# Kernel tuning notes

Hardware: AMD Instinct MI355X
Metric: run time of the kernel (lower is better)

## Reference

```python
import jax, jax.numpy as jnp
import numpy as np

B, D, H1, H2 = 128, 1024, 512, 128


def setup_inputs() -> dict:
    key = jax.random.key(0)
    ks = jax.random.split(key, 5)
    x = jax.random.normal(ks[0], (B, D), dtype=jnp.float32)
    W1 = jax.random.normal(ks[1], (H1, D), dtype=jnp.float32)
    W2 = jax.random.normal(ks[2], (H2, H1), dtype=jnp.float32)
    W3 = jax.random.normal(ks[3], (H1, H2), dtype=jnp.float32)
    W4 = jax.random.normal(ks[4], (D, H1), dtype=jnp.float32)
    b1 = jnp.full((H1,), 0.1, dtype=jnp.float32)
    b2 = jnp.full((H2,), 0.1, dtype=jnp.float32)
    b3 = jnp.full((H1,), 0.1, dtype=jnp.float32)
    b4 = jnp.full((D,), 0.1, dtype=jnp.float32)
    return {"x": x, "W1": W1, "b1": b1, "W2": W2, "b2": b2,
            "W3": W3, "b3": b3, "W4": W4, "b4": b4}


def reference(x, W1, b1, W2, b2, W3, b3, W4, b4):
    # Forward: 4-layer sigmoid autoencoder (calculate_jacobian=True path).
    c1 = jax.nn.sigmoid(x @ W1.T + b1)    # [B, H1]
    c2 = jax.nn.sigmoid(c1 @ W2.T + b2)   # [B, H2]
    c3 = jax.nn.sigmoid(c2 @ W3.T + b3)   # [B, H1]
    recover = c3 @ W4.T + b4              # [B, D]
    # Per-sample Jacobian of recover w.r.t. x, vectorized:
    # diag(sigma') matmul == row-scale, so avoid explicit diag matrices.
    s1 = c1 * (1.0 - c1)                  # [B, H1]
    s2 = c2 * (1.0 - c2)                  # [B, H2]
    s3 = c3 * (1.0 - c3)                  # [B, H1]
    G1 = s1[:, :, None] * W1              # [B, H1, D]
    G2 = jnp.einsum('bi,ij,bjd->bid', s2, W2, G1)   # [B, H2, D]
    G3 = jnp.einsum('bj,ji,bid->bjd', s3, W3, G2)   # [B, H1, D]
    Jac = jnp.einsum('oj,bjd->bod', W4, G3)          # [B, D, D]
    return recover, c2, Jac
```

## Files before the change

kernel.cpp:

```cpp
#include <hip/hip_runtime.h>

#define NB  128
#define ND  1024
#define NH1 512
#define NH2 128

typedef __attribute__((ext_vector_type(8))) short    short8;
typedef __attribute__((ext_vector_type(8))) _Float16 half8;
typedef __attribute__((ext_vector_type(4))) float    f32x4;

__device__ __forceinline__ float sigm(float v) { return 1.0f / (1.0f + __expf(-v)); }

__device__ __forceinline__ void bsplit(float v, unsigned short& h, unsigned short& l) {
    unsigned hu = __float_as_uint(v) & 0xffff0000u;
    h = (unsigned short)(hu >> 16);
    float r = v - __uint_as_float(hu);
    l = (unsigned short)(__float_as_uint(r) >> 16);
}

template<int K, int COLS, bool SIG>
__global__ __launch_bounds__(256)
void fc_kernel(const float* __restrict__ X, const float* __restrict__ W,
               const float* __restrict__ bias, float* __restrict__ Cout,
               float* __restrict__ Sout) {
    int idx4 = blockIdx.x * 256 + threadIdx.x;
    int out = idx4 >> 2, sub = idx4 & 3;
    int r = out / COLS, c = out % COLS;
    constexpr int KQ = K / 4;
    const float4* xr = (const float4*)(X + (long)r * K + sub * KQ);
    const float4* wr = (const float4*)(W + (long)c * K + sub * KQ);
    float acc = 0.f;
#pragma unroll 4
    for (int k = 0; k < KQ / 4; k++) {
        float4 a = xr[k], b = wr[k];
        acc += a.x * b.x + a.y * b.y + a.z * b.z + a.w * b.w;
    }
    acc += __shfl_xor(acc, 1, 64);
    acc += __shfl_xor(acc, 2, 64);
    if (sub == 0) {
        acc += bias[c];
        if (SIG) {
            float cv = sigm(acc);
            Cout[out] = cv;
            Sout[out] = cv * (1.f - cv);
        } else {
            Cout[out] = acc;
        }
    }
}

__global__ __launch_bounds__(256)
void prep_shared(const float* __restrict__ W1, const float* __restrict__ W4,
                 const float* __restrict__ W3,
                 _Float16* __restrict__ W1t16, _Float16* __restrict__ W4_16,
                 float* __restrict__ W3t) {
    int idx = blockIdx.x * 256 + threadIdx.x;
    int d = idx >> 9, j = idx & 511;
    W1t16[idx] = (_Float16)W1[(long)j * ND + d];
    W4_16[idx] = (_Float16)W4[idx];
    if (idx < NH2 * NH1) {
        int i = idx >> 9, jj = idx & 511;
        W3t[idx] = W3[(long)jj * NH2 + i];
    }
}

__global__ __launch_bounds__(256)
void prep_batch(const float* __restrict__ W2, const float* __restrict__ W3t,
                const float* __restrict__ s1, const float* __restrict__ s3,
                _Float16* __restrict__ Br, _Float16* __restrict__ Bl) {
    long idx = (long)blockIdx.x * 256 + threadIdx.x;
    int j = idx & 511;
    int b = idx >> 16;
    int ij = idx & 0xFFFF;
    float s1v = s1[(long)b * NH1 + j];
    float s3v = s3[(long)b * NH1 + j];
    Br[idx] = (_Float16)(W2[ij] * s1v);
    Bl[idx] = (_Float16)(W3t[ij] * s3v);
}

__global__ __launch_bounds__(256)
void mfma_nk2(const _Float16* __restrict__ A0, const _Float16* __restrict__ A1,
              const _Float16* __restrict__ Br, const _Float16* __restrict__ Bl,
              const float* __restrict__ s2,
              unsigned short* __restrict__ Rh, unsigned short* __restrict__ Rl,
              unsigned short* __restrict__ Lh, unsigned short* __restrict__ Ll) {
    int g = blockIdx.x;
    int xcd = g & 7, seq = g >> 3;
    int lb = seq >> 4, inner = seq & 15;
    int b = xcd + 8 * lb;
    int mt = inner & 7, side = inner >> 3;

    const _Float16* A  = side ? A1 : A0;
    const _Float16* Bb = (side ? Bl : Br) + (long)b * NH2 * NH1;
    unsigned short* Oh = (side ? Lh : Rh) + (long)b * ND * NH2;
    unsigned short* Ol = (side ? Ll : Rl) + (long)b * ND * NH2;

    int t = threadIdx.x;
    int lane = t & 63, w = t >> 6;
    int wr = w >> 1, wc = w & 1;
    int m0 = mt * 128 + wr * 64;
    int n0 = wc * 64;
    int lrow = lane & 15;
    int lk   = (lane >> 4) << 3;

    f32x4 zero = {0.f, 0.f, 0.f, 0.f};
    f32x4 acc[4][4];
#pragma unroll
    for (int i = 0; i < 4; i++)
#pragma unroll
        for (int j = 0; j < 4; j++) acc[i][j] = zero;

#pragma unroll 2
    for (int kc = 0; kc < NH1; kc += 32) {
        half8 av[4], bv[4];
#pragma unroll
        for (int i = 0; i < 4; i++) {
            av[i] = *(const half8*)(A  + (long)(m0 + i * 16 + lrow) * NH1 + kc + lk);
            bv[i] = *(const half8*)(Bb + (long)(n0 + i * 16 + lrow) * NH1 + kc + lk);
        }
#pragma unroll
        for (int i = 0; i < 4; i++)
#pragma unroll
            for (int j = 0; j < 4; j++)
                acc[i][j] = __builtin_amdgcn_mfma_f32_16x16x32_f16(av[i], bv[j], acc[i][j], 0, 0, 0);
    }

    float nsc[4] = {1.f, 1.f, 1.f, 1.f};
    if (side) {
#pragma unroll
        for (int j = 0; j < 4; j++) nsc[j] = s2[(long)b * NH2 + n0 + j * 16 + lrow];
    }
    int rbase = (lane >> 4) << 2;
#pragma unroll
    for (int i = 0; i < 4; i++)
#pragma unroll
        for (int r = 0; r < 4; r++) {
            long row = m0 + i * 16 + rbase + r;
#pragma unroll
            for (int j = 0; j < 4; j++) {
                float v = acc[i][j][r] * nsc[j];
                unsigned short h, l;
                bsplit(v, h, l);
                long off = row * NH2 + n0 + j * 16 + lrow;
                Oh[off] = h;
                Ol[off] = l;
            }
        }
}

__global__ __launch_bounds__(256)
void jac_mfma(const unsigned short* __restrict__ Lh, const unsigned short* __restrict__ Ll,
              const unsigned short* __restrict__ Rh, const unsigned short* __restrict__ Rl,
              float* __restrict__ J) {
    int g = blockIdx.x;
    int xcd = g & 7, seq = g >> 3;
    int lb = seq >> 6, inner = seq & 63;
    int b = xcd + 8 * lb;
    int bx = inner & 7, by = inner >> 3;

    long base = (long)b * ((long)ND * NH2);
    const unsigned short* Lhb = Lh + base;
    const unsigned short* Llb = Ll + base;
    const unsigned short* Rhb = Rh + base;
    const unsigned short* Rlb = Rl + base;

    int t = threadIdx.x;
    int lane = t & 63, w = t >> 6;
    int wr = w >> 1, wc = w & 1;
    int m0 = by * 128 + wr * 64;
    int n0 = bx * 128 + wc * 64;
    int lrow = lane & 15;
    int lk   = (lane >> 4) << 3;

    f32x4 zero = {0.f, 0.f, 0.f, 0.f};
    f32x4 acc[4][4];
#pragma unroll
    for (int i = 0; i < 4; i++)
#pragma unroll
        for (int j = 0; j < 4; j++) acc[i][j] = zero;

#pragma unroll
    for (int kc = 0; kc < NH2; kc += 32) {
        short8 ah[4], al[4], bh[4], bl[4];
#pragma unroll
        for (int i = 0; i < 4; i++) {
            long ao = (long)(m0 + i * 16 + lrow) * NH2 + kc + lk;
            ah[i] = *(const short8*)(Lhb + ao);
            al[i] = *(const short8*)(Llb + ao);
            long bo = (long)(n0 + i * 16 + lrow) * NH2 + kc + lk;
            bh[i] = *(const short8*)(Rhb + bo);
            bl[i] = *(const short8*)(Rlb + bo);
        }
#pragma unroll
        for (int i = 0; i < 4; i++)
#pragma unroll
            for (int j = 0; j < 4; j++) {
                acc[i][j] = __builtin_amdgcn_mfma_f32_16x16x32_bf16(ah[i], bh[j], acc[i][j], 0, 0, 0);
                acc[i][j] = __builtin_amdgcn_mfma_f32_16x16x32_bf16(ah[i], bl[j], acc[i][j], 0, 0, 0);
                acc[i][j] = __builtin_amdgcn_mfma_f32_16x16x32_bf16(al[i], bh[j], acc[i][j], 0, 0, 0);
            }
    }

    __shared__ float st[4][16][68];
    float* Jb = J + (long)b * ND * ND;
    int rbase = (lane >> 4) << 2;
#pragma unroll
    for (int i = 0; i < 4; i++) {
#pragma unroll
        for (int j = 0; j < 4; j++)
#pragma unroll
            for (int r = 0; r < 4; r++)
                st[w][rbase + r][j * 16 + lrow] = acc[i][j][r];
#pragma unroll
        for (int q = 0; q < 4; q++) {
            int row  = (lane >> 4) * 4 + q;
            int col4 = (lane & 15) * 4;
            f32x4 v = *(const f32x4*)&st[w][row][col4];
            long off = (long)(m0 + i * 16 + row) * ND + n0 + col4;
            __builtin_nontemporal_store(v, (f32x4*)(Jb + off));
        }
    }
}

extern "C" void kernel_launch(void* const* d_in, const int* in_sizes, int n_in,
                              void* d_out, int out_size, void* d_ws, size_t ws_size,
                              hipStream_t stream) {
    const float* x  = (const float*)d_in[0];
    const float* W1 = (const float*)d_in[1];
    const float* b1 = (const float*)d_in[2];
    const float* W2 = (const float*)d_in[3];
    const float* b2 = (const float*)d_in[4];
    const float* W3 = (const float*)d_in[5];
    const float* b3 = (const float*)d_in[6];
    const float* W4 = (const float*)d_in[7];
    const float* b4 = (const float*)d_in[8];

    float* out_rec = (float*)d_out;
    float* out_c2  = out_rec + NB * ND;
    float* out_jac = out_c2 + NB * NH2;

    float* ws = (float*)d_ws;
    float* c1  = ws;
    float* s1  = c1 + NB * NH1;
    float* s2  = s1 + NB * NH1;
    float* c3  = s2 + NB * NH2;
    float* s3  = c3 + NB * NH1;
    float* W3t = s3 + NB * NH1;
    _Float16* W1t16 = (_Float16*)(W3t + NH2 * NH1);
    _Float16* W4_16 = W1t16 + (long)ND * NH1;
    _Float16* Br    = W4_16 + (long)ND * NH1;
    _Float16* Bl    = Br    + (long)NB * NH2 * NH1;
    unsigned short* Lh = (unsigned short*)(Bl + (long)NB * NH2 * NH1);
    unsigned short* Ll = Lh + (long)NB * ND * NH2;
    unsigned short* Rh = Ll + (long)NB * ND * NH2;
    unsigned short* Rl = Rh + (long)NB * ND * NH2;

    fc_kernel<ND,  NH1, true ><<<NB * NH1 * 4 / 256, 256, 0, stream>>>(x,       W1, b1, c1,      s1);
    fc_kernel<NH1, NH2, true ><<<NB * NH2 * 4 / 256, 256, 0, stream>>>(c1,      W2, b2, out_c2,  s2);
    fc_kernel<NH2, NH1, true ><<<NB * NH1 * 4 / 256, 256, 0, stream>>>(out_c2,  W3, b3, c3,      s3);
    fc_kernel<NH1, ND,  false><<<NB * ND  * 4 / 256, 256, 0, stream>>>(c3,      W4, b4, out_rec, nullptr);

    prep_shared<<<ND * NH1 / 256, 256, 0, stream>>>(W1, W4, W3, W1t16, W4_16, W3t);

    prep_batch<<<(long)NB * NH2 * NH1 / 256, 256, 0, stream>>>(
        W2, W3t, s1, s3, Br, Bl);

    mfma_nk2<<<2048, 256, 0, stream>>>(
        W1t16, W4_16, Br, Bl, s2, Rh, Rl, Lh, Ll);

    jac_mfma<<<8192, 256, 0, stream>>>(Lh, Ll, Rh, Rl, out_jac);
}
```

Measured before the change: 962.6 us.

## Switch GEMMs to 32x32 MFMA, fuse prep into FC launches, vectorize prep

Both MFMA kernels move from 16x16x32 to 32x32x16 instructions with 2x2 tiles per wave, so each wave issues fewer MFMAs and fewer operand loads per output. The epilogue row mapping and the shared staging buffer are resized to match. Weight prep is merged into the fc1 launch and per-batch prep into the fc4 launch, with the per-batch prep vectorized to float4/half4, and fc2/fc3 now split K across 8 lanes instead of 4. This cuts launch count and small-kernel overhead, but the larger staging buffer and bigger accumulator tiles may reduce occupancy.

```diff
diff --git a/kernel.cpp b/kernel.cpp
--- a/kernel.cpp
+++ b/kernel.cpp
@@ -5,9 +5,11 @@
 #define NH1 512
 #define NH2 128
 
-typedef __attribute__((ext_vector_type(8))) short    short8;
-typedef __attribute__((ext_vector_type(8))) _Float16 half8;
-typedef __attribute__((ext_vector_type(4))) float    f32x4;
+typedef __attribute__((ext_vector_type(8)))  short    short8;
+typedef __attribute__((ext_vector_type(8)))  _Float16 half8;
+typedef __attribute__((ext_vector_type(4)))  _Float16 half4;
+typedef __attribute__((ext_vector_type(4)))  float    f32x4;
+typedef __attribute__((ext_vector_type(16))) float    f32x16;
 
 __device__ __forceinline__ float sigm(float v) { return 1.0f / (1.0f + __expf(-v)); }
 
@@ -18,15 +20,14 @@
     l = (unsigned short)(__float_as_uint(r) >> 16);
 }
 
-template<int K, int COLS, bool SIG>
-__global__ __launch_bounds__(256)
-void fc_kernel(const float* __restrict__ X, const float* __restrict__ W,
-               const float* __restrict__ bias, float* __restrict__ Cout,
-               float* __restrict__ Sout) {
-    int idx4 = blockIdx.x * 256 + threadIdx.x;
-    int out = idx4 >> 2, sub = idx4 & 3;
+template<int K, int COLS, bool SIG, int SPLIT>
+__device__ __forceinline__ void fc_body(int bid, const float* __restrict__ X,
+        const float* __restrict__ W, const float* __restrict__ bias,
+        float* __restrict__ Cout, float* __restrict__ Sout) {
+    int idx = bid * 256 + (int)threadIdx.x;
+    int out = idx / SPLIT, sub = idx % SPLIT;
     int r = out / COLS, c = out % COLS;
-    constexpr int KQ = K / 4;
+    constexpr int KQ = K / SPLIT;
     const float4* xr = (const float4*)(X + (long)r * K + sub * KQ);
     const float4* wr = (const float4*)(W + (long)c * K + sub * KQ);
     float acc = 0.f;
@@ -35,8 +36,8 @@
         float4 a = xr[k], b = wr[k];
         acc += a.x * b.x + a.y * b.y + a.z * b.z + a.w * b.w;
     }
-    acc += __shfl_xor(acc, 1, 64);
-    acc += __shfl_xor(acc, 2, 64);
+#pragma unroll
+    for (int o = 1; o < SPLIT; o <<= 1) acc += __shfl_xor(acc, o, 64);
     if (sub == 0) {
         acc += bias[c];
         if (SIG) {
@@ -49,33 +50,62 @@
     }
 }
 
-__global__ __launch_bounds__(256)
-void prep_shared(const float* __restrict__ W1, const float* __restrict__ W4,
-                 const float* __restrict__ W3,
-                 _Float16* __restrict__ W1t16, _Float16* __restrict__ W4_16,
-                 float* __restrict__ W3t) {
-    int idx = blockIdx.x * 256 + threadIdx.x;
-    int d = idx >> 9, j = idx & 511;
-    W1t16[idx] = (_Float16)W1[(long)j * ND + d];
-    W4_16[idx] = (_Float16)W4[idx];
-    if (idx < NH2 * NH1) {
-        int i = idx >> 9, jj = idx & 511;
-        W3t[idx] = W3[(long)jj * NH2 + i];
-    }
-}
-
-__global__ __launch_bounds__(256)
-void prep_batch(const float* __restrict__ W2, const float* __restrict__ W3t,
-                const float* __restrict__ s1, const float* __restrict__ s3,
-                _Float16* __restrict__ Br, _Float16* __restrict__ Bl) {
-    long idx = (long)blockIdx.x * 256 + threadIdx.x;
-    int j = idx & 511;
-    int b = idx >> 16;
-    int ij = idx & 0xFFFF;
-    float s1v = s1[(long)b * NH1 + j];
-    float s3v = s3[(long)b * NH1 + j];
-    Br[idx] = (_Float16)(W2[ij] * s1v);
-    Bl[idx] = (_Float16)(W3t[ij] * s3v);
+template<int K, int COLS, bool SIG, int SPLIT>
+__global__ __launch_bounds__(256)
+void fc_kernel(const float* __restrict__ X, const float* __restrict__ W,
+               const float* __restrict__ bias, float* __restrict__ Cout,
+               float* __restrict__ Sout) {
+    fc_body<K, COLS, SIG, SPLIT>(blockIdx.x, X, W, bias, Cout, Sout);
+}
+
+__global__ __launch_bounds__(256)
+void fc1_prep(const float* __restrict__ x,  const float* __restrict__ W1,
+              const float* __restrict__ b1, float* __restrict__ c1,
+              float* __restrict__ s1,
+              const float* __restrict__ W4, const float* __restrict__ W3,
+              _Float16* __restrict__ W1t16, _Float16* __restrict__ W4_16,
+              float* __restrict__ W3t) {
+    int bid = blockIdx.x;
+    if (bid < NB * NH1 * 4 / 256) {
+        fc_body<ND, NH1, true, 4>(bid, x, W1, b1, c1, s1);
+    } else {
+        int idx = (bid - NB * NH1 * 4 / 256) * 256 + (int)threadIdx.x;
+        int d = idx >> 9, j = idx & 511;
+        W1t16[idx] = (_Float16)W1[(long)j * ND + d];
+        W4_16[idx] = (_Float16)W4[idx];
+        if (idx < NH2 * NH1) {
+            int i = idx >> 9, jj = idx & 511;
+            W3t[idx] = W3[(long)jj * NH2 + i];
+        }
+    }
+}
+
+__global__ __launch_bounds__(256)
+void fc4_prep(const float* __restrict__ c3, const float* __restrict__ W4,
+              const float* __restrict__ b4, float* __restrict__ out_rec,
+              const float* __restrict__ W2, const float* __restrict__ W3t,
+              const float* __restrict__ s1, const float* __restrict__ s3,
+              _Float16* __restrict__ Br, _Float16* __restrict__ Bl) {
+    int bid = blockIdx.x;
+    if (bid < NB * ND * 4 / 256) {
+        fc_body<NH1, ND, false, 4>(bid, c3, W4, b4, out_rec, nullptr);
+    } else {
+        long idx = (long)(bid - NB * ND * 4 / 256) * 256 + threadIdx.x;
+        int j4 = (int)(idx & 127) << 2;
+        int i  = (int)(idx >> 7) & 127;
+        int b  = (int)(idx >> 14);
+        float4 wv = *(const float4*)(W2 + (long)i * NH1 + j4);
+        float4 sv = *(const float4*)(s1 + (long)b * NH1 + j4);
+        half4 o;
+        o[0] = (_Float16)(wv.x * sv.x); o[1] = (_Float16)(wv.y * sv.y);
+        o[2] = (_Float16)(wv.z * sv.z); o[3] = (_Float16)(wv.w * sv.w);
+        *(half4*)(Br + idx * 4) = o;
+        wv = *(const float4*)(W3t + (long)i * NH1 + j4);
+        sv = *(const float4*)(s3  + (long)b * NH1 + j4);
+        o[0] = (_Float16)(wv.x * sv.x); o[1] = (_Float16)(wv.y * sv.y);
+        o[2] = (_Float16)(wv.z * sv.z); o[3] = (_Float16)(wv.w * sv.w);
+        *(half4*)(Bl + idx * 4) = o;
+    }
 }
 
 __global__ __launch_bounds__(256)
@@ -100,52 +130,52 @@
     int wr = w >> 1, wc = w & 1;
     int m0 = mt * 128 + wr * 64;
     int n0 = wc * 64;
-    int lrow = lane & 15;
-    int lk   = (lane >> 4) << 3;
-
-    f32x4 zero = {0.f, 0.f, 0.f, 0.f};
-    f32x4 acc[4][4];
-#pragma unroll
-    for (int i = 0; i < 4; i++)
-#pragma unroll
-        for (int j = 0; j < 4; j++) acc[i][j] = zero;
+    int lrow = lane & 31;
+    int lk   = (lane >> 5) << 3;
+
+    f32x16 acc[2][2];
+#pragma unroll
+    for (int i = 0; i < 2; i++)
+#pragma unroll
+        for (int j = 0; j < 2; j++)
+#pragma unroll
+            for (int r = 0; r < 16; r++) acc[i][j][r] = 0.f;
 
 #pragma unroll 2
-    for (int kc = 0; kc < NH1; kc += 32) {
-        half8 av[4], bv[4];
-#pragma unroll
-        for (int i = 0; i < 4; i++) {
-            av[i] = *(const half8*)(A  + (long)(m0 + i * 16 + lrow) * NH1 + kc + lk);
-            bv[i] = *(const half8*)(Bb + (long)(n0 + i * 16 + lrow) * NH1 + kc + lk);
-        }
-#pragma unroll
-        for (int i = 0; i < 4; i++)
-#pragma unroll
-            for (int j = 0; j < 4; j++)
-                acc[i][j] = __builtin_amdgcn_mfma_f32_16x16x32_f16(av[i], bv[j], acc[i][j], 0, 0, 0);
-    }
-
-    float nsc[4] = {1.f, 1.f, 1.f, 1.f};
+    for (int kc = 0; kc < NH1; kc += 16) {
+        half8 av[2], bv[2];
+#pragma unroll
+        for (int i = 0; i < 2; i++) {
+            av[i] = *(const half8*)(A  + (long)(m0 + i * 32 + lrow) * NH1 + kc + lk);
+            bv[i] = *(const half8*)(Bb + (long)(n0 + i * 32 + lrow) * NH1 + kc + lk);
+        }
+#pragma unroll
+        for (int i = 0; i < 2; i++)
+#pragma unroll
+            for (int j = 0; j < 2; j++)
+                acc[i][j] = __builtin_amdgcn_mfma_f32_32x32x16_f16(av[i], bv[j], acc[i][j], 0, 0, 0);
+    }
+
+    float nsc[2] = {1.f, 1.f};
     if (side) {
 #pragma unroll
-        for (int j = 0; j < 4; j++) nsc[j] = s2[(long)b * NH2 + n0 + j * 16 + lrow];
-    }
-    int rbase = (lane >> 4) << 2;
-#pragma unroll
-    for (int i = 0; i < 4; i++)
-#pragma unroll
-        for (int r = 0; r < 4; r++) {
-            long row = m0 + i * 16 + rbase + r;
-#pragma unroll
-            for (int j = 0; j < 4; j++) {
+        for (int j = 0; j < 2; j++) nsc[j] = s2[(long)b * NH2 + n0 + j * 32 + lrow];
+    }
+    int hi4 = (lane >> 5) << 2;
+#pragma unroll
+    for (int i = 0; i < 2; i++)
+#pragma unroll
+        for (int j = 0; j < 2; j++)
+#pragma unroll
+            for (int r = 0; r < 16; r++) {
+                int row = m0 + i * 32 + (r & 3) + 8 * (r >> 2) + hi4;
                 float v = acc[i][j][r] * nsc[j];
                 unsigned short h, l;
                 bsplit(v, h, l);
-                long off = row * NH2 + n0 + j * 16 + lrow;
+                long off = (long)row * NH2 + n0 + j * 32 + lrow;
                 Oh[off] = h;
                 Ol[off] = l;
             }
-        }
 }
 
 __global__ __launch_bounds__(256)
@@ -169,54 +199,55 @@
     int wr = w >> 1, wc = w & 1;
     int m0 = by * 128 + wr * 64;
     int n0 = bx * 128 + wc * 64;
-    int lrow = lane & 15;
-    int lk   = (lane >> 4) << 3;
-
-    f32x4 zero = {0.f, 0.f, 0.f, 0.f};
-    f32x4 acc[4][4];
-#pragma unroll
-    for (int i = 0; i < 4; i++)
-#pragma unroll
-        for (int j = 0; j < 4; j++) acc[i][j] = zero;
-
-#pragma unroll
-    for (int kc = 0; kc < NH2; kc += 32) {
-        short8 ah[4], al[4], bh[4], bl[4];
-#pragma unroll
-        for (int i = 0; i < 4; i++) {
-            long ao = (long)(m0 + i * 16 + lrow) * NH2 + kc + lk;
+    int lrow = lane & 31;
+    int lk   = (lane >> 5) << 3;
+
+    f32x16 acc[2][2];
+#pragma unroll
+    for (int i = 0; i < 2; i++)
+#pragma unroll
+        for (int j = 0; j < 2; j++)
+#pragma unroll
+            for (int r = 0; r < 16; r++) acc[i][j][r] = 0.f;
+
+#pragma unroll 4
+    for (int kc = 0; kc < NH2; kc += 16) {
+        short8 ah[2], al[2], bh[2], bl[2];
+#pragma unroll
+        for (int i = 0; i < 2; i++) {
+            long ao = (long)(m0 + i * 32 + lrow) * NH2 + kc + lk;
             ah[i] = *(const short8*)(Lhb + ao);
             al[i] = *(const short8*)(Llb + ao);
-            long bo = (long)(n0 + i * 16 + lrow) * NH2 + kc + lk;
+            long bo = (long)(n0 + i * 32 + lrow) * NH2 + kc + lk;
             bh[i] = *(const short8*)(Rhb + bo);
             bl[i] = *(const short8*)(Rlb + bo);
         }
 #pragma unroll
-        for (int i = 0; i < 4; i++)
-#pragma unroll
-            for (int j = 0; j < 4; j++) {
-                acc[i][j] = __builtin_amdgcn_mfma_f32_16x16x32_bf16(ah[i], bh[j], acc[i][j], 0, 0, 0);
-                acc[i][j] = __builtin_amdgcn_mfma_f32_16x16x32_bf16(ah[i], bl[j], acc[i][j], 0, 0, 0);
-                acc[i][j] = __builtin_amdgcn_mfma_f32_16x16x32_bf16(al[i], bh[j], acc[i][j], 0, 0, 0);
+        for (int i = 0; i < 2; i++)
+#pragma unroll
+            for (int j = 0; j < 2; j++) {
+                acc[i][j] = __builtin_amdgcn_mfma_f32_32x32x16_bf16(ah[i], bh[j], acc[i][j], 0, 0, 0);
+                acc[i][j] = __builtin_amdgcn_mfma_f32_32x32x16_bf16(ah[i], bl[j], acc[i][j], 0, 0, 0);
+                acc[i][j] = __builtin_amdgcn_mfma_f32_32x32x16_bf16(al[i], bh[j], acc[i][j], 0, 0, 0);
             }
     }
 
-    __shared__ float st[4][16][68];
+    __shared__ float st[4][32][68];
     float* Jb = J + (long)b * ND * ND;
-    int rbase = (lane >> 4) << 2;
-#pragma unroll
-    for (int i = 0; i < 4; i++) {
-#pragma unroll
-        for (int j = 0; j < 4; j++)
-#pragma unroll
-            for (int r = 0; r < 4; r++)
-                st[w][rbase + r][j * 16 + lrow] = acc[i][j][r];
-#pragma unroll
-        for (int q = 0; q < 4; q++) {
-            int row  = (lane >> 4) * 4 + q;
+    int hi4 = (lane >> 5) << 2;
+#pragma unroll
+    for (int i = 0; i < 2; i++) {
+#pragma unroll
+        for (int j = 0; j < 2; j++)
+#pragma unroll
+            for (int r = 0; r < 16; r++)
+                st[w][(r & 3) + 8 * (r >> 2) + hi4][j * 32 + lrow] = acc[i][j][r];
+#pragma unroll
+        for (int q = 0; q < 8; q++) {
+            int row  = q * 4 + (lane >> 4);
             int col4 = (lane & 15) * 4;
             f32x4 v = *(const f32x4*)&st[w][row][col4];
-            long off = (long)(m0 + i * 16 + row) * ND + n0 + col4;
+            long off = (long)(m0 + i * 32 + row) * ND + n0 + col4;
             __builtin_nontemporal_store(v, (f32x4*)(Jb + off));
         }
     }
@@ -255,15 +286,14 @@
     unsigned short* Rh = Ll + (long)NB * ND * NH2;
     unsigned short* Rl = Rh + (long)NB * ND * NH2;
 
-    fc_kernel<ND,  NH1, true ><<<NB * NH1 * 4 / 256, 256, 0, stream>>>(x,       W1, b1, c1,      s1);
-    fc_kernel<NH1, NH2, true ><<<NB * NH2 * 4 / 256, 256, 0, stream>>>(c1,      W2, b2, out_c2,  s2);
-    fc_kernel<NH2, NH1, true ><<<NB * NH1 * 4 / 256, 256, 0, stream>>>(out_c2,  W3, b3, c3,      s3);
-    fc_kernel<NH1, ND,  false><<<NB * ND  * 4 / 256, 256, 0, stream>>>(c3,      W4, b4, out_rec, nullptr);
-
-    prep_shared<<<ND * NH1 / 256, 256, 0, stream>>>(W1, W4, W3, W1t16, W4_16, W3t);
-
-    prep_batch<<<(long)NB * NH2 * NH1 / 256, 256, 0, stream>>>(
-        W2, W3t, s1, s3, Br, Bl);
+    fc1_prep<<<NB * NH1 * 4 / 256 + ND * NH1 / 256, 256, 0, stream>>>(
+        x, W1, b1, c1, s1, W4, W3, W1t16, W4_16, W3t);
+
+    fc_kernel<NH1, NH2, true, 8><<<NB * NH2 * 8 / 256, 256, 0, stream>>>(c1,     W2, b2, out_c2, s2);
+    fc_kernel<NH2, NH1, true, 8><<<NB * NH1 * 8 / 256, 256, 0, stream>>>(out_c2, W3, b3, c3,     s3);
+
+    fc4_prep<<<NB * ND * 4 / 256 + (long)NB * NH2 * NH1 / 1024, 256, 0, stream>>>(
+        c3, W4, b4, out_rec, W2, W3t, s1, s3, Br, Bl);
 
     mfma_nk2<<<2048, 256, 0, stream>>>(
         W1t16, W4_16, Br, Bl, s2, Rh, Rl, Lh, Ll);
```

Result: no change. 953.5 us (-0.9%).
